# Kernel optimization log

Measured on AMD Instinct MI355X. Metric: run time of the kernel, lower is better.

Reference implementation:

```python
import jax, jax.numpy as jnp
import numpy as np

HEADS = 8
DIM_HEAD = 64
QUERY_DIM = 512
INNER = HEADS * DIM_HEAD
T = 16
MAX_REL = 16  # == temporal_length
SCALE = DIM_HEAD ** -0.5


def _rel_idx(length_q, length_k):
    rq = jnp.arange(length_q)
    rk = jnp.arange(length_k)
    dist = rk[None, :] - rq[:, None]
    return jnp.clip(dist, -MAX_REL, MAX_REL) + MAX_REL  # [Tq, Tk] in [0, 2*MAX_REL]


def setup_inputs() -> dict:
    key = jax.random.key(0)
    ks = jax.random.split(key, 8)
    B = 2048
    s = 0.02
    return {
        "x": jax.random.normal(ks[0], (B, T, QUERY_DIM), dtype=jnp.float32),
        "Wq": jax.random.normal(ks[1], (QUERY_DIM, INNER), dtype=jnp.float32) * s,
        "Wk": jax.random.normal(ks[2], (QUERY_DIM, INNER), dtype=jnp.float32) * s,
        "Wv": jax.random.normal(ks[3], (QUERY_DIM, INNER), dtype=jnp.float32) * s,
        "Wo": jax.random.normal(ks[4], (INNER, QUERY_DIM), dtype=jnp.float32) * s,
        "bo": jnp.zeros((QUERY_DIM,), dtype=jnp.float32),
        "rel_k_table": jax.random.normal(ks[5], (2 * MAX_REL + 1, DIM_HEAD), dtype=jnp.float32) * s,
        "rel_v_table": jax.random.normal(ks[6], (2 * MAX_REL + 1, DIM_HEAD), dtype=jnp.float32) * s,
    }


def reference(x, Wq, Wk, Wv, Wo, bo, rel_k_table, rel_v_table):
    B, N, _ = x.shape
    # projections (Linear without bias)
    def split_heads(t):
        return t.reshape(B, N, HEADS, DIM_HEAD).transpose(0, 2, 1, 3)  # [B, H, N, D]
    q = split_heads(x @ Wq)
    k = split_heads(x @ Wk)
    v = split_heads(x @ Wv)

    sim = jnp.einsum('bhid,bhjd->bhij', q, k) * SCALE
    idx = _rel_idx(N, N)                     # [N, N]
    k2 = rel_k_table[idx]                    # [N, N, D]
    sim = sim + jnp.einsum('bhtd,tsd->bhts', q, k2) * SCALE

    attn = jax.nn.softmax(sim, axis=-1)
    out = jnp.einsum('bhij,bhjd->bhid', attn, v)
    v2 = rel_v_table[idx]                    # [N, N, D]
    out = out + jnp.einsum('bhts,tsd->bhtd', attn, v2)

    out = out.transpose(0, 2, 1, 3).reshape(B, N, INNER)
    return out @ Wo + bo
```

## Files before the change

### kernel.cpp

```cpp
#include <hip/hip_runtime.h>
#include <stdint.h>


using bf16x8 = __attribute__((ext_vector_type(8))) short;
using f32x4  = __attribute__((ext_vector_type(4))) float;

#define AS3P(p) ((__attribute__((address_space(3))) void*)(p))
#define AS1P(p) ((const __attribute__((address_space(1))) void*)(p))

__device__ __forceinline__ uint16_t f2bf(float f) {
  unsigned int x = __builtin_bit_cast(unsigned int, f);
  x += 0x7fffu + ((x >> 16) & 1u);
  return (uint16_t)(x >> 16);
}

__global__ void cast_kernel(const float* __restrict__ in, uint16_t* __restrict__ out, int n8) {
  int i = blockIdx.x * 256 + threadIdx.x;
  if (i >= n8) return;
  float4 a = ((const float4*)in)[i * 2];
  float4 b = ((const float4*)in)[i * 2 + 1];
  uint4 r;
  r.x = (uint32_t)f2bf(a.x) | ((uint32_t)f2bf(a.y) << 16);
  r.y = (uint32_t)f2bf(a.z) | ((uint32_t)f2bf(a.w) << 16);
  r.z = (uint32_t)f2bf(b.x) | ((uint32_t)f2bf(b.y) << 16);
  r.w = (uint32_t)f2bf(b.z) | ((uint32_t)f2bf(b.w) << 16);
  ((uint4*)out)[i] = r;
}

__global__ void transpose_cast4(const float* __restrict__ Wq, const float* __restrict__ Wk,
                                const float* __restrict__ Wv, const float* __restrict__ Wo,
                                uint16_t* __restrict__ WqkvT, uint16_t* __restrict__ WoT) {
  __shared__ float tile[32][33];
  const int z = blockIdx.z;
  const float* src = (z == 0) ? Wq : (z == 1) ? Wk : (z == 2) ? Wv : Wo;
  uint16_t* dst = (z == 3) ? WoT : (WqkvT + z * 262144);
  int tx = threadIdx.x, ty = threadIdx.y;
  int c0 = blockIdx.x * 32, r0 = blockIdx.y * 32;
  #pragma unroll
  for (int k = 0; k < 4; ++k)
    tile[ty + 8 * k][tx] = src[(r0 + ty + 8 * k) * 512 + c0 + tx];
  __syncthreads();
  #pragma unroll
  for (int k = 0; k < 4; ++k)
    dst[(c0 + ty + 8 * k) * 512 + r0 + tx] = f2bf(tile[tx][ty + 8 * k]);
}

template<int OUT_MODE, int KDIM>
__global__ __launch_bounds__(512, 2) void gemm256(
    const uint16_t* __restrict__ A, const uint16_t* __restrict__ B,
    void* __restrict__ C, const float* __restrict__ bias, int N, int nbx) {
  constexpr int NT = KDIM / 32;
  __shared__ __align__(16) uint16_t lds[4][2][8192];
  __shared__ __align__(16) uint16_t ldsO[8][1024];
  const int tid = threadIdx.x;
  const int w = tid >> 6, l = tid & 63;
  const int lr = l & 15, kc = l >> 4;
  const int wm = w >> 2, wn = w & 3;
  const int cpx = gridDim.x >> 3;
  const int id = blockIdx.x;
  const int swz = (id & 7) * cpx + (id >> 3);
  const int by = swz / nbx, bx = swz - by * nbx;
  const int mBase = by * 256, nBase = bx * 256;
  const int g8 = l >> 3;
  const int sub = (l & 7) ^ g8;
  const int srow = w * 32 + g8 * 2 + (sub >> 2);
  const int scol = (sub & 3) * 8;
  const uint16_t* gA0 = A + (size_t)(mBase + srow) * KDIM + scol;
  const uint16_t* gA1 = gA0 + 16 * KDIM;
  const uint16_t* gB0 = B + (size_t)(nBase + srow) * KDIM + scol;
  const uint16_t* gB1 = gB0 + 16 * KDIM;
  int offA[8], offB[4];
  #pragma unroll
  for (int m = 0; m < 8; ++m) {
    int row = wm * 128 + m * 16 + lr;
    int rp = row >> 1, sb = ((row & 1) << 2) | kc;
    offA[m] = rp * 128 + ((sb ^ (rp & 7)) << 4);
  }
  #pragma unroll
  for (int n = 0; n < 4; ++n) {
    int row = wn * 64 + n * 16 + lr;
    int rp = row >> 1, sb = ((row & 1) << 2) | kc;
    offB[n] = rp * 128 + ((sb ^ (rp & 7)) << 4);
  }
  f32x4 acc[8][4] = {};
  #pragma unroll
  for (int pt = 0; pt < 3; ++pt) {
    uint16_t* dA = &lds[pt][0][w * 1024];
    uint16_t* dB = &lds[pt][1][w * 1024];
    __builtin_amdgcn_global_load_lds(AS1P(gA0 + pt * 32), AS3P(dA),       16, 0, 0);
    __builtin_amdgcn_global_load_lds(AS1P(gA1 + pt * 32), AS3P(dA + 512), 16, 0, 0);
    __builtin_amdgcn_global_load_lds(AS1P(gB0 + pt * 32), AS3P(dB),       16, 0, 0);
    __builtin_amdgcn_global_load_lds(AS1P(gB1 + pt * 32), AS3P(dB + 512), 16, 0, 0);
  }
  asm volatile("s_waitcnt vmcnt(8)" ::: "memory");
  __builtin_amdgcn_s_barrier();
  #pragma unroll 4
  for (int t = 0; t < NT; ++t) {
    const int bi = t & 3;
    const int si = (t + 3) & 3;
    const char* bufA = (const char*)&lds[bi][0][0];
    const char* bufB = (const char*)&lds[bi][1][0];
    if (t + 3 < NT) {
      uint16_t* dA = &lds[si][0][w * 1024];
      __builtin_amdgcn_global_load_lds(AS1P(gA0 + (t + 3) * 32), AS3P(dA),       16, 0, 0);
      __builtin_amdgcn_global_load_lds(AS1P(gA1 + (t + 3) * 32), AS3P(dA + 512), 16, 0, 0);
    }
    if (t + 3 < NT)       asm volatile("s_waitcnt vmcnt(6)" ::: "memory");
    else if (t + 3 == NT) asm volatile("s_waitcnt vmcnt(4)" ::: "memory");
    else if (t + 2 == NT) asm volatile("s_waitcnt vmcnt(0)" ::: "memory");
    bf16x8 a0 = *(const bf16x8*)(bufA + offA[0]);
    bf16x8 a1 = *(const bf16x8*)(bufA + offA[1]);
    bf16x8 a2 = *(const bf16x8*)(bufA + offA[2]);
    bf16x8 a3 = *(const bf16x8*)(bufA + offA[3]);
    bf16x8 b0 = *(const bf16x8*)(bufB + offB[0]);
    bf16x8 b1 = *(const bf16x8*)(bufB + offB[1]);
    bf16x8 b2 = *(const bf16x8*)(bufB + offB[2]);
    bf16x8 b3 = *(const bf16x8*)(bufB + offB[3]);
    __builtin_amdgcn_sched_barrier(0);
    __builtin_amdgcn_s_barrier();
    asm volatile("s_waitcnt lgkmcnt(0)" ::: "memory");
    __builtin_amdgcn_sched_barrier(0);
    __builtin_amdgcn_s_setprio(1);
    acc[0][0] = __builtin_amdgcn_mfma_f32_16x16x32_bf16(a0, b0, acc[0][0], 0, 0, 0);
    acc[0][1] = __builtin_amdgcn_mfma_f32_16x16x32_bf16(a0, b1, acc[0][1], 0, 0, 0);
    acc[0][2] = __builtin_amdgcn_mfma_f32_16x16x32_bf16(a0, b2, acc[0][2], 0, 0, 0);
    acc[0][3] = __builtin_amdgcn_mfma_f32_16x16x32_bf16(a0, b3, acc[0][3], 0, 0, 0);
    acc[1][0] = __builtin_amdgcn_mfma_f32_16x16x32_bf16(a1, b0, acc[1][0], 0, 0, 0);
    acc[1][1] = __builtin_amdgcn_mfma_f32_16x16x32_bf16(a1, b1, acc[1][1], 0, 0, 0);
    acc[1][2] = __builtin_amdgcn_mfma_f32_16x16x32_bf16(a1, b2, acc[1][2], 0, 0, 0);
    acc[1][3] = __builtin_amdgcn_mfma_f32_16x16x32_bf16(a1, b3, acc[1][3], 0, 0, 0);
    acc[2][0] = __builtin_amdgcn_mfma_f32_16x16x32_bf16(a2, b0, acc[2][0], 0, 0, 0);
    acc[2][1] = __builtin_amdgcn_mfma_f32_16x16x32_bf16(a2, b1, acc[2][1], 0, 0, 0);
    acc[2][2] = __builtin_amdgcn_mfma_f32_16x16x32_bf16(a2, b2, acc[2][2], 0, 0, 0);
    acc[2][3] = __builtin_amdgcn_mfma_f32_16x16x32_bf16(a2, b3, acc[2][3], 0, 0, 0);
    acc[3][0] = __builtin_amdgcn_mfma_f32_16x16x32_bf16(a3, b0, acc[3][0], 0, 0, 0);
    acc[3][1] = __builtin_amdgcn_mfma_f32_16x16x32_bf16(a3, b1, acc[3][1], 0, 0, 0);
    acc[3][2] = __builtin_amdgcn_mfma_f32_16x16x32_bf16(a3, b2, acc[3][2], 0, 0, 0);
    acc[3][3] = __builtin_amdgcn_mfma_f32_16x16x32_bf16(a3, b3, acc[3][3], 0, 0, 0);
    __builtin_amdgcn_s_setprio(0);
    __builtin_amdgcn_sched_barrier(0);
    __builtin_amdgcn_s_barrier();
    if (t + 3 < NT) {
      uint16_t* dB = &lds[si][1][w * 1024];
      __builtin_amdgcn_global_load_lds(AS1P(gB0 + (t + 3) * 32), AS3P(dB),       16, 0, 0);
      __builtin_amdgcn_global_load_lds(AS1P(gB1 + (t + 3) * 32), AS3P(dB + 512), 16, 0, 0);
    }
    bf16x8 a4 = *(const bf16x8*)(bufA + offA[4]);
    bf16x8 a5 = *(const bf16x8*)(bufA + offA[5]);
    bf16x8 a6 = *(const bf16x8*)(bufA + offA[6]);
    bf16x8 a7 = *(const bf16x8*)(bufA + offA[7]);
    __builtin_amdgcn_sched_barrier(0);
    __builtin_amdgcn_s_barrier();
    asm volatile("s_waitcnt lgkmcnt(0)" ::: "memory");
    __builtin_amdgcn_sched_barrier(0);
    __builtin_amdgcn_s_setprio(1);
    acc[4][0] = __builtin_amdgcn_mfma_f32_16x16x32_bf16(a4, b0, acc[4][0], 0, 0, 0);
    acc[4][1] = __builtin_amdgcn_mfma_f32_16x16x32_bf16(a4, b1, acc[4][1], 0, 0, 0);
    acc[4][2] = __builtin_amdgcn_mfma_f32_16x16x32_bf16(a4, b2, acc[4][2], 0, 0, 0);
    acc[4][3] = __builtin_amdgcn_mfma_f32_16x16x32_bf16(a4, b3, acc[4][3], 0, 0, 0);
    acc[5][0] = __builtin_amdgcn_mfma_f32_16x16x32_bf16(a5, b0, acc[5][0], 0, 0, 0);
    acc[5][1] = __builtin_amdgcn_mfma_f32_16x16x32_bf16(a5, b1, acc[5][1], 0, 0, 0);
    acc[5][2] = __builtin_amdgcn_mfma_f32_16x16x32_bf16(a5, b2, acc[5][2], 0, 0, 0);
    acc[5][3] = __builtin_amdgcn_mfma_f32_16x16x32_bf16(a5, b3, acc[5][3], 0, 0, 0);
    acc[6][0] = __builtin_amdgcn_mfma_f32_16x16x32_bf16(a6, b0, acc[6][0], 0, 0, 0);
    acc[6][1] = __builtin_amdgcn_mfma_f32_16x16x32_bf16(a6, b1, acc[6][1], 0, 0, 0);
    acc[6][2] = __builtin_amdgcn_mfma_f32_16x16x32_bf16(a6, b2, acc[6][2], 0, 0, 0);
    acc[6][3] = __builtin_amdgcn_mfma_f32_16x16x32_bf16(a6, b3, acc[6][3], 0, 0, 0);
    acc[7][0] = __builtin_amdgcn_mfma_f32_16x16x32_bf16(a7, b0, acc[7][0], 0, 0, 0);
    acc[7][1] = __builtin_amdgcn_mfma_f32_16x16x32_bf16(a7, b1, acc[7][1], 0, 0, 0);
    acc[7][2] = __builtin_amdgcn_mfma_f32_16x16x32_bf16(a7, b2, acc[7][2], 0, 0, 0);
    acc[7][3] = __builtin_amdgcn_mfma_f32_16x16x32_bf16(a7, b3, acc[7][3], 0, 0, 0);
    __builtin_amdgcn_s_setprio(0);
    __builtin_amdgcn_sched_barrier(0);
    __builtin_amdgcn_s_barrier();
  }
  if (OUT_MODE == 1) {
    uint16_t* oW = &ldsO[w][0];
    const int t2 = l >> 3, c2 = l & 7;
    const int grp = bx * 4 + wn;
    const int z = grp >> 3, h = grp & 7;
    uint16_t* gO = (uint16_t*)C + (size_t)h * 6291456 +
                   (size_t)(mBase + wm * 128 + t2) * 192 + z * 64 + c2 * 8;
    #pragma unroll
    for (int m = 0; m < 8; ++m) {
      #pragma unroll
      for (int n = 0; n < 4; ++n)
        #pragma unroll
        for (int r = 0; r < 4; ++r) {
          const int tt = kc * 4 + r;
          const int d = n * 16 + lr;
          const int col = (((d >> 3) ^ (tt & 7)) << 3) | (d & 7);
          oW[tt * 64 + col] = f2bf(acc[m][n][r]);
        }
      asm volatile("s_waitcnt lgkmcnt(0)" ::: "memory");
      __builtin_amdgcn_sched_barrier(0);
      bf16x8 s0 = *(const bf16x8*)(oW + t2 * 64 + (((c2 ^ (t2 & 7)) << 3)));
      bf16x8 s1 = *(const bf16x8*)(oW + (8 + t2) * 64 + (((c2 ^ (t2 & 7)) << 3)));
      *(bf16x8*)(gO + (size_t)(m * 16) * 192) = s0;
      *(bf16x8*)(gO + (size_t)(m * 16 + 8) * 192) = s1;
      asm volatile("s_waitcnt lgkmcnt(0)" ::: "memory");
      __builtin_amdgcn_sched_barrier(0);
    }
  } else {
    #pragma unroll
    for (int m = 0; m < 8; ++m)
      #pragma unroll
      for (int n = 0; n < 4; ++n) {
        const int col = nBase + wn * 64 + n * 16 + lr;
        #pragma unroll
        for (int r = 0; r < 4; ++r) {
          const int row = mBase + wm * 128 + m * 16 + kc * 4 + r;
          ((float*)C)[(size_t)row * N + col] = acc[m][n][r] + bias[col];
        }
      }
  }
}

__global__ __launch_bounds__(512) void attn_kernel(
    const uint16_t* __restrict__ qkv,
    const float* __restrict__ relk, const float* __restrict__ relv,
    uint16_t* __restrict__ outA) {
  __shared__ __align__(16) uint16_t relkS[33 * 72];
  __shared__ __align__(16) uint16_t relvT[64 * 40];
  __shared__ __align__(16) uint16_t vT[8][64 * 24];
  __shared__ float attnS[8][16 * 17];
  const int tid = threadIdx.x;
  for (int e = tid; e < 33 * 64; e += 512) {
    int j = e >> 6, d = e & 63;
    relkS[j * 72 + d] = f2bf(relk[e]);
    relvT[d * 40 + j] = f2bf(relv[e]);
  }
  const int w = tid >> 6, l = tid & 63;
  const int bh = blockIdx.x * 8 + w;
  const int b = bh >> 3, h = bh & 7;
  const int lr = l & 15, kc = l >> 4;
  const uint16_t* base = qkv + (size_t)h * 6291456 + (size_t)(b * 16) * 192;
  const uint16_t* qrow = base + lr * 192;
  bf16x8 aq0 = *(const bf16x8*)(qrow + kc * 8);
  bf16x8 aq1 = *(const bf16x8*)(qrow + 32 + kc * 8);
  const uint16_t* krow = qrow + 64;
  bf16x8 bk0 = *(const bf16x8*)(krow + kc * 8);
  bf16x8 bk1 = *(const bf16x8*)(krow + 32 + kc * 8);
  {
    const int s = l >> 2, dg = l & 3;
    const uint16_t* vrow = base + s * 192 + 128 + dg * 16;
    uint4 v0 = *(const uint4*)vrow;
    uint4 v1 = *(const uint4*)(vrow + 8);
    uint16_t tmp[16];
    *(uint4*)(tmp) = v0; *(uint4*)(tmp + 8) = v1;
    #pragma unroll
    for (int i = 0; i < 16; ++i)
      vT[w][(dg * 16 + i) * 24 + s] = tmp[i];
  }
  __syncthreads();
  const f32x4 zero = {0.f, 0.f, 0.f, 0.f};
  f32x4 sim = __builtin_amdgcn_mfma_f32_16x16x32_bf16(aq0, bk0, zero, 0, 0, 0);
  sim = __builtin_amdgcn_mfma_f32_16x16x32_bf16(aq1, bk1, sim, 0, 0, 0);
  bf16x8 rka0 = *(const bf16x8*)(relkS + lr * 72 + kc * 8);
  bf16x8 rka1 = *(const bf16x8*)(relkS + lr * 72 + 32 + kc * 8);
  bf16x8 rkb0 = *(const bf16x8*)(relkS + (16 + lr) * 72 + kc * 8);
  bf16x8 rkb1 = *(const bf16x8*)(relkS + (16 + lr) * 72 + 32 + kc * 8);
  f32x4 rqa = __builtin_amdgcn_mfma_f32_16x16x32_bf16(aq0, rka0, zero, 0, 0, 0);
  rqa = __builtin_amdgcn_mfma_f32_16x16x32_bf16(aq1, rka1, rqa, 0, 0, 0);
  f32x4 rqb = __builtin_amdgcn_mfma_f32_16x16x32_bf16(aq0, rkb0, zero, 0, 0, 0);
  rqb = __builtin_amdgcn_mfma_f32_16x16x32_bf16(aq1, rkb1, rqb, 0, 0, 0);
  #pragma unroll
  for (int r = 0; r < 4; ++r) {
    const int t = kc * 4 + r;
    const int j = lr - t + 16;
    const int src = (l & 48) | (j & 15);
    const float va = __shfl(rqa[r], src, 64);
    const float vb = __shfl(rqb[r], src, 64);
    const float rqv = (j < 16) ? va : vb;
    float sv = (sim[r] + rqv) * 0.125f;
    float m = sv;
    m = fmaxf(m, __shfl_xor(m, 1, 64));
    m = fmaxf(m, __shfl_xor(m, 2, 64));
    m = fmaxf(m, __shfl_xor(m, 4, 64));
    m = fmaxf(m, __shfl_xor(m, 8, 64));
    const float p = __expf(sv - m);
    float su = p;
    su += __shfl_xor(su, 1, 64);
    su += __shfl_xor(su, 2, 64);
    su += __shfl_xor(su, 4, 64);
    su += __shfl_xor(su, 8, 64);
    attnS[w][t * 17 + lr] = p / su;
  }
  __syncthreads();
  const float* aS = attnS[w];
  bf16x8 attnA, w2A;
  #pragma unroll
  for (int i = 0; i < 8; ++i) {
    const int s1 = kc * 8 + i;
    attnA[i] = (s1 < 16) ? (short)f2bf(aS[lr * 17 + s1]) : (short)0;
    const int s2 = s1 + lr - 16;
    w2A[i] = (s2 >= 0 && s2 < 16) ? (short)f2bf(aS[lr * 17 + s2]) : (short)0;
  }
  f32x4 o[4];
  #pragma unroll
  for (int dt = 0; dt < 4; ++dt) {
    bf16x8 vf  = *(const bf16x8*)(&vT[w][(dt * 16 + lr) * 24 + (kc & 1) * 8]);
    bf16x8 rvf = *(const bf16x8*)(&relvT[(dt * 16 + lr) * 40 + kc * 8]);
    o[dt] = __builtin_amdgcn_mfma_f32_16x16x32_bf16(w2A, rvf, zero, 0, 0, 0);
    o[dt] = __builtin_amdgcn_mfma_f32_16x16x32_bf16(attnA, vf, o[dt], 0, 0, 0);
  }
  asm volatile("s_waitcnt lgkmcnt(0)" ::: "memory");
  __builtin_amdgcn_sched_barrier(0);
  uint16_t* oW = &vT[w][0];
  #pragma unroll
  for (int dt = 0; dt < 4; ++dt)
    #pragma unroll
    for (int r = 0; r < 4; ++r) {
      const int t = kc * 4 + r;
      const int chunk = dt * 2 + (lr >> 3);
      oW[t * 64 + ((chunk ^ (t & 7)) << 3) + (lr & 7)] = f2bf(o[dt][r]);
    }
  asm volatile("s_waitcnt lgkmcnt(0)" ::: "memory");
  __builtin_amdgcn_sched_barrier(0);
  const int t2 = l >> 3, c2 = l & 7;
  bf16x8 s0 = *(const bf16x8*)(oW + t2 * 64 + ((c2 ^ (t2 & 7)) << 3));
  bf16x8 s1 = *(const bf16x8*)(oW + (8 + t2) * 64 + ((c2 ^ (t2 & 7)) << 3));
  *(bf16x8*)(outA + (size_t)(b * 16 + t2) * 512 + h * 64 + c2 * 8) = s0;
  *(bf16x8*)(outA + (size_t)(b * 16 + 8 + t2) * 512 + h * 64 + c2 * 8) = s1;
}

extern "C" void kernel_launch(void* const* d_in, const int* in_sizes, int n_in,
                              void* d_out, int out_size, void* d_ws, size_t ws_size,
                              hipStream_t stream) {
  const float* x    = (const float*)d_in[0];
  const float* Wq   = (const float*)d_in[1];
  const float* Wk   = (const float*)d_in[2];
  const float* Wv   = (const float*)d_in[3];
  const float* Wo   = (const float*)d_in[4];
  const float* bo   = (const float*)d_in[5];
  const float* relk = (const float*)d_in[6];
  const float* relv = (const float*)d_in[7];

  char* ws = (char*)d_ws;
  uint16_t* qkv   = (uint16_t*)ws;
  uint16_t* xbf   = (uint16_t*)(ws + 100663296);
  uint16_t* WqkvT = (uint16_t*)(ws + 134217728);
  uint16_t* WoT   = (uint16_t*)(ws + 135790592);
  uint16_t* attnO = xbf;

  cast_kernel<<<8192, 256, 0, stream>>>(x, xbf, 2097152);
  transpose_cast4<<<dim3(16, 16, 4), dim3(32, 8), 0, stream>>>(Wq, Wk, Wv, Wo, WqkvT, WoT);
  gemm256<1, 512><<<dim3(768), dim3(512), 0, stream>>>(xbf, WqkvT, (void*)qkv, nullptr, 1536, 6);
  attn_kernel<<<2048, 512, 0, stream>>>(qkv, relk, relv, attnO);
  gemm256<0, 512><<<dim3(256), dim3(512), 0, stream>>>(attnO, WoT, d_out, bo, 512, 2);
}
```

Baseline: 143.6 us.

## Shrink GEMM tile to 256x128 with 4 waves and 3-stage LDS pipeline

The GEMM kernel now runs 256 threads (4 waves in a 2x2 layout) on a 256x128 output tile instead of 512 threads on 256x256, which doubles the grid for both the QKV and output projections. The LDS ring drops from 4 buffers to 3 with prefetch distance 2, and the staging loads are restructured into macros so each wave loads 64 A rows and 32 B rows. The aim is more blocks for better CU fill and less LDS per block. In exchange, operand reuse per tile is lower and the pipeline is shallower, so more global traffic and possible latency exposure.

```diff
diff --git a/kernel.cpp b/kernel.cpp
--- a/kernel.cpp
+++ b/kernel.cpp
@@ -46,29 +46,26 @@
 }
 
 template<int OUT_MODE, int KDIM>
-__global__ __launch_bounds__(512, 2) void gemm256(
+__global__ __launch_bounds__(256, 2) void gemm256(
     const uint16_t* __restrict__ A, const uint16_t* __restrict__ B,
     void* __restrict__ C, const float* __restrict__ bias, int N, int nbx) {
   constexpr int NT = KDIM / 32;
-  __shared__ __align__(16) uint16_t lds[4][2][8192];
-  __shared__ __align__(16) uint16_t ldsO[8][1024];
+  __shared__ __align__(16) uint16_t ldsA[3][8192];
+  __shared__ __align__(16) uint16_t ldsB[3][4096];
+  __shared__ __align__(16) uint16_t ldsO[4][1024];
   const int tid = threadIdx.x;
   const int w = tid >> 6, l = tid & 63;
   const int lr = l & 15, kc = l >> 4;
-  const int wm = w >> 2, wn = w & 3;
+  const int wm = w >> 1, wn = w & 1;
   const int cpx = gridDim.x >> 3;
   const int id = blockIdx.x;
   const int swz = (id & 7) * cpx + (id >> 3);
   const int by = swz / nbx, bx = swz - by * nbx;
-  const int mBase = by * 256, nBase = bx * 256;
+  const int mBase = by * 256, nBase = bx * 128;
   const int g8 = l >> 3;
   const int sub = (l & 7) ^ g8;
-  const int srow = w * 32 + g8 * 2 + (sub >> 2);
-  const int scol = (sub & 3) * 8;
-  const uint16_t* gA0 = A + (size_t)(mBase + srow) * KDIM + scol;
-  const uint16_t* gA1 = gA0 + 16 * KDIM;
-  const uint16_t* gB0 = B + (size_t)(nBase + srow) * KDIM + scol;
-  const uint16_t* gB1 = gB0 + 16 * KDIM;
+  const uint16_t* gA = A + (size_t)(mBase + w * 64 + g8 * 2 + (sub >> 2)) * KDIM + (sub & 3) * 8;
+  const uint16_t* gB = B + (size_t)(nBase + w * 32 + g8 * 2 + (sub >> 2)) * KDIM + (sub & 3) * 8;
   int offA[8], offB[4];
   #pragma unroll
   for (int m = 0; m < 8; ++m) {
@@ -83,31 +80,36 @@
     offB[n] = rp * 128 + ((sb ^ (rp & 7)) << 4);
   }
   f32x4 acc[8][4] = {};
-  #pragma unroll
-  for (int pt = 0; pt < 3; ++pt) {
-    uint16_t* dA = &lds[pt][0][w * 1024];
-    uint16_t* dB = &lds[pt][1][w * 1024];
-    __builtin_amdgcn_global_load_lds(AS1P(gA0 + pt * 32), AS3P(dA),       16, 0, 0);
-    __builtin_amdgcn_global_load_lds(AS1P(gA1 + pt * 32), AS3P(dA + 512), 16, 0, 0);
-    __builtin_amdgcn_global_load_lds(AS1P(gB0 + pt * 32), AS3P(dB),       16, 0, 0);
-    __builtin_amdgcn_global_load_lds(AS1P(gB1 + pt * 32), AS3P(dB + 512), 16, 0, 0);
-  }
-  asm volatile("s_waitcnt vmcnt(8)" ::: "memory");
+
+#define STAGE_A(t, bf) do { \
+    uint16_t* d = &ldsA[bf][w * 2048]; \
+    const uint16_t* s = gA + (t) * 32; \
+    __builtin_amdgcn_global_load_lds(AS1P(s),              AS3P(d),        16, 0, 0); \
+    __builtin_amdgcn_global_load_lds(AS1P(s + 16 * KDIM),  AS3P(d + 512),  16, 0, 0); \
+    __builtin_amdgcn_global_load_lds(AS1P(s + 32 * KDIM),  AS3P(d + 1024), 16, 0, 0); \
+    __builtin_amdgcn_global_load_lds(AS1P(s + 48 * KDIM),  AS3P(d + 1536), 16, 0, 0); \
+  } while (0)
+#define STAGE_B(t, bf) do { \
+    uint16_t* d = &ldsB[bf][w * 1024]; \
+    const uint16_t* s = gB + (t) * 32; \
+    __builtin_amdgcn_global_load_lds(AS1P(s),              AS3P(d),        16, 0, 0); \
+    __builtin_amdgcn_global_load_lds(AS1P(s + 16 * KDIM),  AS3P(d + 512),  16, 0, 0); \
+  } while (0)
+
+  STAGE_A(0, 0); STAGE_B(0, 0);
+  STAGE_A(1, 1); STAGE_B(1, 1);
+  asm volatile("s_waitcnt vmcnt(6)" ::: "memory");
   __builtin_amdgcn_s_barrier();
-  #pragma unroll 4
+
+  #pragma unroll
   for (int t = 0; t < NT; ++t) {
-    const int bi = t & 3;
-    const int si = (t + 3) & 3;
-    const char* bufA = (const char*)&lds[bi][0][0];
-    const char* bufB = (const char*)&lds[bi][1][0];
-    if (t + 3 < NT) {
-      uint16_t* dA = &lds[si][0][w * 1024];
-      __builtin_amdgcn_global_load_lds(AS1P(gA0 + (t + 3) * 32), AS3P(dA),       16, 0, 0);
-      __builtin_amdgcn_global_load_lds(AS1P(gA1 + (t + 3) * 32), AS3P(dA + 512), 16, 0, 0);
-    }
-    if (t + 3 < NT)       asm volatile("s_waitcnt vmcnt(6)" ::: "memory");
-    else if (t + 3 == NT) asm volatile("s_waitcnt vmcnt(4)" ::: "memory");
-    else if (t + 2 == NT) asm volatile("s_waitcnt vmcnt(0)" ::: "memory");
+    const int bi = t % 3;
+    const int si = (t + 2) % 3;
+    const char* bufA = (const char*)&ldsA[bi][0];
+    const char* bufB = (const char*)&ldsB[bi][0];
+    if (t + 2 < NT) STAGE_A(t + 2, si);
+    if (t + 2 < NT) asm volatile("s_waitcnt vmcnt(4)" ::: "memory");
+    else            asm volatile("s_waitcnt vmcnt(0)" ::: "memory");
     bf16x8 a0 = *(const bf16x8*)(bufA + offA[0]);
     bf16x8 a1 = *(const bf16x8*)(bufA + offA[1]);
     bf16x8 a2 = *(const bf16x8*)(bufA + offA[2]);
@@ -140,11 +142,7 @@
     __builtin_amdgcn_s_setprio(0);
     __builtin_amdgcn_sched_barrier(0);
     __builtin_amdgcn_s_barrier();
-    if (t + 3 < NT) {
-      uint16_t* dB = &lds[si][1][w * 1024];
-      __builtin_amdgcn_global_load_lds(AS1P(gB0 + (t + 3) * 32), AS3P(dB),       16, 0, 0);
-      __builtin_amdgcn_global_load_lds(AS1P(gB1 + (t + 3) * 32), AS3P(dB + 512), 16, 0, 0);
-    }
+    if (t + 2 < NT) STAGE_B(t + 2, si);
     bf16x8 a4 = *(const bf16x8*)(bufA + offA[4]);
     bf16x8 a5 = *(const bf16x8*)(bufA + offA[5]);
     bf16x8 a6 = *(const bf16x8*)(bufA + offA[6]);
@@ -174,10 +172,12 @@
     __builtin_amdgcn_sched_barrier(0);
     __builtin_amdgcn_s_barrier();
   }
+#undef STAGE_A
+#undef STAGE_B
   if (OUT_MODE == 1) {
     uint16_t* oW = &ldsO[w][0];
     const int t2 = l >> 3, c2 = l & 7;
-    const int grp = bx * 4 + wn;
+    const int grp = bx * 2 + wn;
     const int z = grp >> 3, h = grp & 7;
     uint16_t* gO = (uint16_t*)C + (size_t)h * 6291456 +
                    (size_t)(mBase + wm * 128 + t2) * 192 + z * 64 + c2 * 8;
@@ -345,7 +345,7 @@
 
   cast_kernel<<<8192, 256, 0, stream>>>(x, xbf, 2097152);
   transpose_cast4<<<dim3(16, 16, 4), dim3(32, 8), 0, stream>>>(Wq, Wk, Wv, Wo, WqkvT, WoT);
-  gemm256<1, 512><<<dim3(768), dim3(512), 0, stream>>>(xbf, WqkvT, (void*)qkv, nullptr, 1536, 6);
+  gemm256<1, 512><<<dim3(1536), dim3(256), 0, stream>>>(xbf, WqkvT, (void*)qkv, nullptr, 1536, 12);
   attn_kernel<<<2048, 512, 0, stream>>>(qkv, relk, relv, attnO);
-  gemm256<0, 512><<<dim3(256), dim3(512), 0, stream>>>(attnO, WoT, d_out, bo, 512, 2);
-}
+  gemm256<0, 512><<<dim3(512), dim3(256), 0, stream>>>(attnO, WoT, d_out, bo, 512, 4);
+}
```

Measured after the change: 140.2 us (median of 3 runs). 2.4% less time.
